# Kernel tuning notes

Hardware: AMD Instinct MI355X
Metric: run time of the kernel (lower is better)

Reference implementation:

```python
import jax, jax.numpy as jnp
import numpy as np

D = 256      # d_model
NH = 8       # num_heads
NP = 4       # n_points
H = 100      # feature map height (single level)
W = 100      # feature map width
B = 4
Q = H * W
S = H * W


def setup_inputs() -> dict:
    key = jax.random.key(0)
    ks = jax.random.split(key, 12)
    p = lambda k, shp, s=0.02: jax.random.normal(k, shp, jnp.float32) * s
    return {
        "hidden_states": jax.random.normal(ks[0], (B, Q, D), jnp.float32),
        "encoder_hidden_states": jax.random.normal(ks[1], (B, S, D), jnp.float32),
        "reference_points": jax.random.uniform(ks[2], (B, Q, 1, 2), jnp.float32),
        "spatial_shapes": jnp.array([[H, W]], dtype=jnp.int32),
        "W_off": p(ks[3], (NH * NP * 2, D)),
        "b_off": p(ks[4], (NH * NP * 2,), 0.5),
        "W_attn": p(ks[5], (NH * NP, D)),
        "b_attn": jnp.zeros((NH * NP,), jnp.float32),
        "W_val": p(ks[6], (D, D)),
        "b_val": jnp.zeros((D,), jnp.float32),
        "W_out": p(ks[7], (D, D)),
        "b_out": jnp.zeros((D,), jnp.float32),
    }


def _deform_attn(hidden_states, encoder_hidden_states, reference_points,
                 W_off, b_off, W_attn, b_attn, W_val, b_val, W_out, b_out):
    Bsz, Qn, Dm = hidden_states.shape
    d = Dm // NH

    # value projection -> [B, NH, S, d]
    value = (encoder_hidden_states @ W_val.T + b_val).reshape(Bsz, S, NH, d)
    vflat = value.transpose(0, 2, 1, 3).reshape(Bsz * NH, H * W, d)

    # sampling offsets [B,Q,NH,NP,2] (n_levels=1 squeezed)
    off = (hidden_states @ W_off.T + b_off).reshape(Bsz, Qn, NH, NP, 2)
    # attention weights softmax over (n_levels*n_points)=NP -> [B,Q,NH,NP]
    attn = jax.nn.softmax((hidden_states @ W_attn.T + b_attn).reshape(Bsz, Qn, NH, NP), axis=-1)

    # normalized sampling locations: ref + off / [W, H]
    normalizer = jnp.array([W, H], jnp.float32)
    # reference_points: [B,Q,1,2] (level dim) -> broadcast over heads/points
    loc = reference_points[:, :, None, 0, None, :] + off / normalizer  # [B,Q,NH,NP,2]

    # grid_sample semantics: grid = 2*loc - 1, align_corners=False, zeros padding
    gx = 2.0 * loc[..., 0] - 1.0
    gy = 2.0 * loc[..., 1] - 1.0
    x = ((gx + 1.0) * W - 1.0) * 0.5   # pixel coords [B,Q,NH,NP]
    y = ((gy + 1.0) * H - 1.0) * 0.5
    x0 = jnp.floor(x); y0 = jnp.floor(y)
    x1 = x0 + 1.0;     y1 = y0 + 1.0
    wx1 = x - x0; wx0 = 1.0 - wx1
    wy1 = y - y0; wy0 = 1.0 - wy1

    bh = jnp.arange(Bsz * NH)[:, None]

    def corner(xi, yi, wgt):
        valid = (xi >= 0) & (xi <= W - 1) & (yi >= 0) & (yi <= H - 1)
        xi_c = jnp.clip(xi, 0, W - 1).astype(jnp.int32)
        yi_c = jnp.clip(yi, 0, H - 1).astype(jnp.int32)
        idx = (yi_c * W + xi_c).transpose(0, 2, 1, 3).reshape(Bsz * NH, Qn * NP)
        g = vflat[bh, idx]  # [B*NH, Q*NP, d]
        wv = (wgt * valid.astype(wgt.dtype)).transpose(0, 2, 1, 3).reshape(Bsz * NH, Qn * NP, 1)
        return g * wv

    sampled = corner(x0, y0, wx0 * wy0)
    sampled = sampled + corner(x1, y0, wx1 * wy0)
    sampled = sampled + corner(x0, y1, wx0 * wy1)
    sampled = sampled + corner(x1, y1, wx1 * wy1)
    sampled = sampled.reshape(Bsz, NH, Qn, NP, d)

    out = jnp.einsum("bhqpd,bqhp->bqhd", sampled, attn).reshape(Bsz, Qn, Dm)
    return out @ W_out.T + b_out


def reference(hidden_states, encoder_hidden_states, reference_points, spatial_shapes,
              W_off, b_off, W_attn, b_attn, W_val, b_val, W_out, b_out):
    # spatial_shapes is static metadata (must equal [[H, W]]); shapes are baked in.
    return _deform_attn(hidden_states, encoder_hidden_states, reference_points,
                        W_off, b_off, W_attn, b_attn, W_val, b_val, W_out, b_out)
```

## Files before the change

kernel.cpp:

```cpp
#include <hip/hip_runtime.h>

constexpr int HH = 100;
constexpr int WW = 100;
constexpr int NH = 8;
constexpr int NP = 4;
constexpr int B  = 4;
constexpr int Q  = HH * WW;
constexpr int S  = Q;
constexpr int K  = 256;
constexpr int DH = 32;

typedef __attribute__((ext_vector_type(8))) short short8;
typedef __attribute__((ext_vector_type(4))) float f32x4;

struct ushort4_t { unsigned short x, y, z, w; };

__device__ inline unsigned short f2bf(float f) {
    unsigned u = __builtin_bit_cast(unsigned, f);
    u += 0x7fffu + ((u >> 16) & 1u);
    return (unsigned short)(u >> 16);
}
__device__ inline float bf2f(unsigned short h) {
    return __builtin_bit_cast(float, ((unsigned)h) << 16);
}

__device__ inline void lds_store16(short* base, int row, int kcol, short8 v) {
    const int idx = row * 64 + (kcol ^ ((row & 7) << 3));
    *reinterpret_cast<short8*>(&base[idx]) = v;
}
__device__ inline short8 lds_load16(const short* base, int row, int kcol) {
    const int idx = row * 64 + (kcol ^ ((row & 7) << 3));
    return *reinterpret_cast<const short8*>(&base[idx]);
}

__device__ inline short8 cvt8(float4 a, float4 b) {
    short8 r;
    r[0] = (short)f2bf(a.x); r[1] = (short)f2bf(a.y);
    r[2] = (short)f2bf(a.z); r[3] = (short)f2bf(a.w);
    r[4] = (short)f2bf(b.x); r[5] = (short)f2bf(b.y);
    r[6] = (short)f2bf(b.z); r[7] = (short)f2bf(b.w);
    return r;
}

template <int MODE, int NT>
__global__ __launch_bounds__(512) void gemm_mfma(
    const void* __restrict__ Ap, const float* __restrict__ W0,
    const float* __restrict__ W1, const float* __restrict__ b0,
    const float* __restrict__ b1, void* __restrict__ Cp, int N0)
{
    constexpr int BROWS = (NT + 63) / 64;

    __shared__ short As[64 * 64];
    __shared__ short Bs[NT * 64];

    const int tid  = threadIdx.x;
    const int m0   = blockIdx.x * 64;
    const int lane = tid & 63;
    const int w    = tid >> 6;
    const int l15  = lane & 15;
    const int l4   = lane >> 4;
    const int srow = tid >> 3;
    const int sk8  = (tid & 7) * 8;

    const int n_base = (MODE == 1) ? w * 16 : w * 32;
    constexpr int NF = (MODE == 1) ? 1 : 2;

    f32x4 acc[4][2];
#pragma unroll
    for (int i = 0; i < 4; ++i)
#pragma unroll
        for (int j = 0; j < 2; ++j)
            acc[i][j] = f32x4{0.f, 0.f, 0.f, 0.f};

    float4 fa0, fa1;
    short8 sa;
    float4 fb[BROWS][2];

    auto load_tile = [&](int k0) {
        if constexpr (MODE == 2) {
            const unsigned short* A = (const unsigned short*)Ap;
            sa = *reinterpret_cast<const short8*>(&A[(size_t)(m0 + srow) * K + k0 + sk8]);
        } else {
            const float* A = (const float*)Ap;
            const float* s = &A[(size_t)(m0 + srow) * K + k0 + sk8];
            fa0 = *reinterpret_cast<const float4*>(s);
            fa1 = *reinterpret_cast<const float4*>(s + 4);
        }
#pragma unroll
        for (int i = 0; i < BROWS; ++i) {
            const int row = srow + 64 * i;
            if ((NT % 64 == 0) || row < NT) {
                const float* s = (row < N0)
                    ? &W0[(size_t)row * K + k0 + sk8]
                    : &W1[(size_t)(row - N0) * K + k0 + sk8];
                fb[i][0] = *reinterpret_cast<const float4*>(s);
                fb[i][1] = *reinterpret_cast<const float4*>(s + 4);
            }
        }
    };
    auto write_lds = [&]() {
        if constexpr (MODE == 2) {
            lds_store16(As, srow, sk8, sa);
        } else {
            lds_store16(As, srow, sk8, cvt8(fa0, fa1));
        }
#pragma unroll
        for (int i = 0; i < BROWS; ++i) {
            const int row = srow + 64 * i;
            if ((NT % 64 == 0) || row < NT)
                lds_store16(Bs, row, sk8, cvt8(fb[i][0], fb[i][1]));
        }
    };

    load_tile(0);
    for (int k0 = 0; k0 < K; k0 += 64) {
        write_lds();
        __syncthreads();
        if (k0 + 64 < K) load_tile(k0 + 64);
        if (n_base < NT) {
#pragma unroll
            for (int kk = 0; kk < 2; ++kk) {
                const int kc = kk * 32 + l4 * 8;
                short8 a[4];
#pragma unroll
                for (int mf = 0; mf < 4; ++mf)
                    a[mf] = lds_load16(As, mf * 16 + l15, kc);
#pragma unroll
                for (int nf = 0; nf < NF; ++nf) {
                    const short8 bv = lds_load16(Bs, n_base + nf * 16 + l15, kc);
#pragma unroll
                    for (int mf = 0; mf < 4; ++mf)
                        acc[mf][nf] = __builtin_amdgcn_mfma_f32_16x16x32_bf16(
                            a[mf], bv, acc[mf][nf], 0, 0, 0);
                }
            }
        }
        __syncthreads();
    }

#pragma unroll
    for (int nf = 0; nf < NF; ++nf) {
        const int n = n_base + nf * 16 + l15;
        if (n >= NT) continue;
        const float bias = (n < N0) ? b0[n] : b1[n - N0];
#pragma unroll
        for (int mf = 0; mf < 4; ++mf) {
#pragma unroll
            for (int r = 0; r < 4; ++r) {
                const int m = m0 + mf * 16 + l4 * 4 + r;
                const float v = acc[mf][nf][r] + bias;
                if constexpr (MODE == 0) {
                    const int b = m / S, s = m - (m / S) * S;
                    const int h = n >> 5, dd = n & 31;
                    ((unsigned short*)Cp)[(((size_t)(b * NH + h)) * S + s) * DH + dd] = f2bf(v);
                } else if constexpr (MODE == 1) {
                    ((float*)Cp)[(size_t)m * 96 + n] = v;
                } else {
                    ((float*)Cp)[(size_t)m * 256 + n] = v;
                }
            }
        }
    }
}

__global__ __launch_bounds__(256) void sample_agg(
    const unsigned short* __restrict__ vflat,
    const float* __restrict__ proj,
    const float* __restrict__ ref,
    unsigned short* __restrict__ tmp)
{
    const int nblk = gridDim.x;
    const int cpx  = nblk >> 3;
    const int swz  = (blockIdx.x & 7) * cpx + (blockIdx.x >> 3);

    const int lg   = threadIdx.x >> 3;
    const int lane = threadIdx.x & 7;
    const int d0   = lane * 4;

    const int g  = swz * 32 + lg;
    const int q  = g % Q;
    const int bh = g / Q;
    const int b  = bh >> 3;
    const int h  = bh & 7;

    const size_t bq   = (size_t)b * Q + q;
    const float refx = ref[bq * 2 + 0];
    const float refy = ref[bq * 2 + 1];
    const float* pr = proj + bq * 96;

    float l[NP];
#pragma unroll
    for (int p = 0; p < NP; ++p) l[p] = pr[64 + h * 4 + p];
    const float mx = fmaxf(fmaxf(l[0], l[1]), fmaxf(l[2], l[3]));
    float e[NP];
    float esum = 0.f;
#pragma unroll
    for (int p = 0; p < NP; ++p) { e[p] = __expf(l[p] - mx); esum += e[p]; }
    const float inv = 1.f / esum;

    const unsigned short* vbase = vflat + (size_t)bh * (S * DH);

    int   cidx[NP][4];
    float cw[NP][4];
#pragma unroll
    for (int p = 0; p < NP; ++p) {
        const float ox = pr[h * 8 + p * 2 + 0];
        const float oy = pr[h * 8 + p * 2 + 1];
        const float x = (refx + ox * (1.0f / WW)) * WW - 0.5f;
        const float y = (refy + oy * (1.0f / HH)) * HH - 0.5f;
        const float x0f = floorf(x);
        const float y0f = floorf(y);
        const float wx1 = x - x0f, wx0 = 1.f - wx1;
        const float wy1 = y - y0f, wy0 = 1.f - wy1;
        const int x0 = (int)x0f;
        const int y0 = (int)y0f;
        const bool vx0 = (x0 >= 0) && (x0 <= WW - 1);
        const bool vx1 = (x0 + 1 >= 0) && (x0 + 1 <= WW - 1);
        const bool vy0 = (y0 >= 0) && (y0 <= HH - 1);
        const bool vy1 = (y0 + 1 >= 0) && (y0 + 1 <= HH - 1);
        const int xi0 = min(max(x0, 0), WW - 1);
        const int xi1 = min(max(x0 + 1, 0), WW - 1);
        const int yi0 = min(max(y0, 0), HH - 1);
        const int yi1 = min(max(y0 + 1, 0), HH - 1);
        const float ap = e[p] * inv;
        cw[p][0] = ap * wx0 * wy0 * ((vx0 && vy0) ? 1.f : 0.f);
        cw[p][1] = ap * wx1 * wy0 * ((vx1 && vy0) ? 1.f : 0.f);
        cw[p][2] = ap * wx0 * wy1 * ((vx0 && vy1) ? 1.f : 0.f);
        cw[p][3] = ap * wx1 * wy1 * ((vx1 && vy1) ? 1.f : 0.f);
        cidx[p][0] = (yi0 * WW + xi0) * DH + d0;
        cidx[p][1] = (yi0 * WW + xi1) * DH + d0;
        cidx[p][2] = (yi1 * WW + xi0) * DH + d0;
        cidx[p][3] = (yi1 * WW + xi1) * DH + d0;
    }

    float a0 = 0.f, a1 = 0.f, a2 = 0.f, a3 = 0.f;
#pragma unroll
    for (int p = 0; p < NP; ++p) {
#pragma unroll
        for (int c = 0; c < 4; ++c) {
            const ushort4_t v = *reinterpret_cast<const ushort4_t*>(&vbase[cidx[p][c]]);
            const float wgt = cw[p][c];
            a0 = fmaf(wgt, bf2f(v.x), a0);
            a1 = fmaf(wgt, bf2f(v.y), a1);
            a2 = fmaf(wgt, bf2f(v.z), a2);
            a3 = fmaf(wgt, bf2f(v.w), a3);
        }
    }

    ushort4_t o;
    o.x = f2bf(a0); o.y = f2bf(a1); o.z = f2bf(a2); o.w = f2bf(a3);
    *reinterpret_cast<ushort4_t*>(&tmp[bq * 256 + h * 32 + d0]) = o;
}

extern "C" void kernel_launch(void* const* d_in, const int* in_sizes, int n_in,
                              void* d_out, int out_size, void* d_ws, size_t ws_size,
                              hipStream_t stream)
{
    const float* hidden = (const float*)d_in[0];
    const float* enc    = (const float*)d_in[1];
    const float* refp   = (const float*)d_in[2];
    const float* W_off  = (const float*)d_in[4];
    const float* b_off  = (const float*)d_in[5];
    const float* W_attn = (const float*)d_in[6];
    const float* b_attn = (const float*)d_in[7];
    const float* W_val  = (const float*)d_in[8];
    const float* b_val  = (const float*)d_in[9];
    const float* W_out  = (const float*)d_in[10];
    const float* b_out  = (const float*)d_in[11];
    float* out = (float*)d_out;

    unsigned short* vflat = (unsigned short*)d_ws;
    float* proj = (float*)((char*)d_ws + (size_t)B * NH * S * DH * 2);
    unsigned short* tmp = (unsigned short*)((char*)proj + (size_t)B * Q * 96 * 4);

    const int M = B * Q;

    gemm_mfma<0, 256><<<M / 64, 512, 0, stream>>>(
        (const void*)enc, W_val, W_val, b_val, b_val, (void*)vflat, 256);

    gemm_mfma<1, 96><<<M / 64, 512, 0, stream>>>(
        (const void*)hidden, W_off, W_attn, b_off, b_attn, (void*)proj, 64);

    sample_agg<<<(B * NH * Q) / 32, 256, 0, stream>>>(vflat, proj, refp, tmp);

    gemm_mfma<2, 256><<<M / 64, 512, 0, stream>>>(
        (const void*)tmp, W_out, W_out, b_out, b_out, (void*)out, 256);
}
```

Baseline: 89.46 us.

## Rewrite GEMMs as persistent LDS-resident-weight kernels with bf16 weight preconversion

Adds a kernel that converts all weight matrices to bf16 once, then replaces the three tiled GEMM launches with persistent 1024-thread kernels. Each of these loads the full weight matrix into LDS once and loops over 32-row tiles of activations, prefetching the next tile. The offset/attention projection output is stored in fp16 instead of fp32 to halve its traffic. The sampling kernel now loads 8 channels per thread with 16-byte reads. Risks include lower occupancy from the large LDS footprint, serialized tile loops, and fp16 precision loss on the sampling offsets.

```diff
diff --git a/kernel.cpp b/kernel.cpp
--- a/kernel.cpp
+++ b/kernel.cpp
@@ -9,11 +9,13 @@
 constexpr int S  = Q;
 constexpr int K  = 256;
 constexpr int DH = 32;
+constexpr int M  = B * Q;
+constexpr int NTILES = M / 32;
 
 typedef __attribute__((ext_vector_type(8))) short short8;
 typedef __attribute__((ext_vector_type(4))) float f32x4;
 
-struct ushort4_t { unsigned short x, y, z, w; };
+struct __align__(8) ushort4_t { unsigned short x, y, z, w; };
 
 __device__ inline unsigned short f2bf(float f) {
     unsigned u = __builtin_bit_cast(unsigned, f);
@@ -23,14 +25,19 @@
 __device__ inline float bf2f(unsigned short h) {
     return __builtin_bit_cast(float, ((unsigned)h) << 16);
 }
-
-__device__ inline void lds_store16(short* base, int row, int kcol, short8 v) {
-    const int idx = row * 64 + (kcol ^ ((row & 7) << 3));
-    *reinterpret_cast<short8*>(&base[idx]) = v;
-}
-__device__ inline short8 lds_load16(const short* base, int row, int kcol) {
-    const int idx = row * 64 + (kcol ^ ((row & 7) << 3));
-    return *reinterpret_cast<const short8*>(&base[idx]);
+__device__ inline unsigned short f2h(float f) {
+    _Float16 h = (_Float16)f;
+    return __builtin_bit_cast(unsigned short, h);
+}
+__device__ inline float h2f(unsigned short u) {
+    return (float)__builtin_bit_cast(_Float16, u);
+}
+
+__device__ inline void lds_st16s(short* base, int row, int stride, int kcol, short8 v) {
+    *reinterpret_cast<short8*>(&base[row * stride + (kcol ^ ((row & 7) << 3))]) = v;
+}
+__device__ inline short8 lds_ld16s(const short* base, int row, int stride, int kcol) {
+    return *reinterpret_cast<const short8*>(&base[row * stride + (kcol ^ ((row & 7) << 3))]);
 }
 
 __device__ inline short8 cvt8(float4 a, float4 b) {
@@ -42,130 +49,155 @@
     return r;
 }
 
-template <int MODE, int NT>
-__global__ __launch_bounds__(512) void gemm_mfma(
-    const void* __restrict__ Ap, const float* __restrict__ W0,
-    const float* __restrict__ W1, const float* __restrict__ b0,
-    const float* __restrict__ b1, void* __restrict__ Cp, int N0)
-{
-    constexpr int BROWS = (NT + 63) / 64;
-
-    __shared__ short As[64 * 64];
-    __shared__ short Bs[NT * 64];
+__global__ __launch_bounds__(256) void preconv(
+    const float* __restrict__ wval, const float* __restrict__ woff,
+    const float* __restrict__ wattn, const float* __restrict__ wo,
+    unsigned short* __restrict__ wbf)
+{
+    const int i4 = (blockIdx.x * 256 + threadIdx.x) * 4;
+    const float* src;
+    if (i4 < 65536) {
+        src = wval + i4;
+    } else if (i4 < 90112) {
+        const int local = i4 - 65536;
+        src = (local < 16384) ? woff + local : wattn + (local - 16384);
+    } else {
+        src = wo + (i4 - 90112);
+    }
+    const float4 f = *reinterpret_cast<const float4*>(src);
+    ushort4_t o;
+    o.x = f2bf(f.x); o.y = f2bf(f.y); o.z = f2bf(f.z); o.w = f2bf(f.w);
+    *reinterpret_cast<ushort4_t*>(&wbf[i4]) = o;
+}
+
+__global__ __launch_bounds__(1024) void value_persist(
+    const float* __restrict__ enc, const unsigned short* __restrict__ wbf,
+    const float* __restrict__ bias, unsigned short* __restrict__ vflat)
+{
+    __shared__ short Bs[256 * 256];
+    __shared__ short As[32 * 256];
 
     const int tid  = threadIdx.x;
-    const int m0   = blockIdx.x * 64;
-    const int lane = tid & 63;
-    const int w    = tid >> 6;
-    const int l15  = lane & 15;
-    const int l4   = lane >> 4;
-    const int srow = tid >> 3;
-    const int sk8  = (tid & 7) * 8;
-
-    const int n_base = (MODE == 1) ? w * 16 : w * 32;
-    constexpr int NF = (MODE == 1) ? 1 : 2;
-
-    f32x4 acc[4][2];
-#pragma unroll
-    for (int i = 0; i < 4; ++i)
-#pragma unroll
-        for (int j = 0; j < 2; ++j)
-            acc[i][j] = f32x4{0.f, 0.f, 0.f, 0.f};
-
+    const int lane = tid & 63, w = tid >> 6;
+    const int l15  = lane & 15, l4 = lane >> 4;
+
+    const int arow = tid >> 5, ak = (tid & 31) * 8;
+
+    int t = blockIdx.x;
     float4 fa0, fa1;
-    short8 sa;
-    float4 fb[BROWS][2];
-
-    auto load_tile = [&](int k0) {
-        if constexpr (MODE == 2) {
-            const unsigned short* A = (const unsigned short*)Ap;
-            sa = *reinterpret_cast<const short8*>(&A[(size_t)(m0 + srow) * K + k0 + sk8]);
-        } else {
-            const float* A = (const float*)Ap;
-            const float* s = &A[(size_t)(m0 + srow) * K + k0 + sk8];
-            fa0 = *reinterpret_cast<const float4*>(s);
-            fa1 = *reinterpret_cast<const float4*>(s + 4);
-        }
-#pragma unroll
-        for (int i = 0; i < BROWS; ++i) {
-            const int row = srow + 64 * i;
-            if ((NT % 64 == 0) || row < NT) {
-                const float* s = (row < N0)
-                    ? &W0[(size_t)row * K + k0 + sk8]
-                    : &W1[(size_t)(row - N0) * K + k0 + sk8];
-                fb[i][0] = *reinterpret_cast<const float4*>(s);
-                fb[i][1] = *reinterpret_cast<const float4*>(s + 4);
+    auto lda = [&](int tt) {
+        const float* s = &enc[(size_t)(tt * 32 + arow) * K + ak];
+        fa0 = *reinterpret_cast<const float4*>(s);
+        fa1 = *reinterpret_cast<const float4*>(s + 4);
+    };
+    lda(t);
+
+    {
+        const int brow = tid >> 2, kb = (tid & 3) * 64;
+#pragma unroll
+        for (int c = 0; c < 8; ++c) {
+            short8 v = *reinterpret_cast<const short8*>(&wbf[brow * 256 + kb + c * 8]);
+            lds_st16s(Bs, brow, 256, kb + c * 8, v);
+        }
+    }
+
+    const int nb = w * 16;
+    const int n = nb + l15;
+    const float bv = bias[n];
+    const int h = n >> 5, dd = n & 31;
+
+    for (; t < NTILES; t += 256) {
+        lds_st16s(As, arow, 256, ak, cvt8(fa0, fa1));
+        __syncthreads();
+        if (t + 256 < NTILES) lda(t + 256);
+
+        f32x4 acc0 = {0.f, 0.f, 0.f, 0.f}, acc1 = {0.f, 0.f, 0.f, 0.f};
+#pragma unroll
+        for (int ks = 0; ks < 8; ++ks) {
+            const int kc = ks * 32 + l4 * 8;
+            const short8 bb = lds_ld16s(Bs, n, 256, kc);
+            const short8 a0 = lds_ld16s(As, l15, 256, kc);
+            const short8 a1 = lds_ld16s(As, 16 + l15, 256, kc);
+            acc0 = __builtin_amdgcn_mfma_f32_16x16x32_bf16(a0, bb, acc0, 0, 0, 0);
+            acc1 = __builtin_amdgcn_mfma_f32_16x16x32_bf16(a1, bb, acc1, 0, 0, 0);
+        }
+        const int m0 = t * 32;
+#pragma unroll
+        for (int r = 0; r < 4; ++r) {
+            int m = m0 + l4 * 4 + r;
+            int b_ = m / S, s_ = m - b_ * S;
+            vflat[(((size_t)(b_ * NH + h)) * S + s_) * DH + dd] = f2bf(acc0[r] + bv);
+            m += 16; b_ = m / S; s_ = m - b_ * S;
+            vflat[(((size_t)(b_ * NH + h)) * S + s_) * DH + dd] = f2bf(acc1[r] + bv);
+        }
+        __syncthreads();
+    }
+}
+
+__global__ __launch_bounds__(1024) void proj_persist(
+    const float* __restrict__ hidden, const unsigned short* __restrict__ wbf,
+    const float* __restrict__ boff, const float* __restrict__ battn,
+    unsigned short* __restrict__ proj)
+{
+    __shared__ short Bs[96 * 256];
+    __shared__ short As[32 * 256];
+
+    const int tid  = threadIdx.x;
+    const int lane = tid & 63, w = tid >> 6;
+    const int l15  = lane & 15, l4 = lane >> 4;
+
+    const int arow = tid >> 5, ak = (tid & 31) * 8;
+
+    int t = blockIdx.x;
+    float4 fa0, fa1;
+    auto lda = [&](int tt) {
+        const float* s = &hidden[(size_t)(tt * 32 + arow) * K + ak];
+        fa0 = *reinterpret_cast<const float4*>(s);
+        fa1 = *reinterpret_cast<const float4*>(s + 4);
+    };
+    lda(t);
+
+    {
+#pragma unroll
+        for (int j = 0; j < 3; ++j) {
+            const int ch = tid * 3 + j;
+            const int brow = ch >> 5, kc = (ch & 31) * 8;
+            short8 v = *reinterpret_cast<const short8*>(&wbf[brow * 256 + kc]);
+            lds_st16s(Bs, brow, 256, kc, v);
+        }
+    }
+
+    const int nf = w >> 1, mh = w & 1;
+    const int n = nf * 16 + l15;
+    const float bv = (w < 12) ? ((n < 64) ? boff[n] : battn[n - 64]) : 0.f;
+
+    for (; t < NTILES; t += 512) {
+        lds_st16s(As, arow, 256, ak, cvt8(fa0, fa1));
+        __syncthreads();
+        if (t + 512 < NTILES) lda(t + 512);
+
+        if (w < 12) {
+            f32x4 acc = {0.f, 0.f, 0.f, 0.f};
+#pragma unroll
+            for (int ks = 0; ks < 8; ++ks) {
+                const int kc = ks * 32 + l4 * 8;
+                const short8 bb = lds_ld16s(Bs, n, 256, kc);
+                const short8 a = lds_ld16s(As, mh * 16 + l15, 256, kc);
+                acc = __builtin_amdgcn_mfma_f32_16x16x32_bf16(a, bb, acc, 0, 0, 0);
             }
-        }
-    };
-    auto write_lds = [&]() {
-        if constexpr (MODE == 2) {
-            lds_store16(As, srow, sk8, sa);
-        } else {
-            lds_store16(As, srow, sk8, cvt8(fa0, fa1));
-        }
-#pragma unroll
-        for (int i = 0; i < BROWS; ++i) {
-            const int row = srow + 64 * i;
-            if ((NT % 64 == 0) || row < NT)
-                lds_store16(Bs, row, sk8, cvt8(fb[i][0], fb[i][1]));
-        }
-    };
-
-    load_tile(0);
-    for (int k0 = 0; k0 < K; k0 += 64) {
-        write_lds();
-        __syncthreads();
-        if (k0 + 64 < K) load_tile(k0 + 64);
-        if (n_base < NT) {
-#pragma unroll
-            for (int kk = 0; kk < 2; ++kk) {
-                const int kc = kk * 32 + l4 * 8;
-                short8 a[4];
-#pragma unroll
-                for (int mf = 0; mf < 4; ++mf)
-                    a[mf] = lds_load16(As, mf * 16 + l15, kc);
-#pragma unroll
-                for (int nf = 0; nf < NF; ++nf) {
-                    const short8 bv = lds_load16(Bs, n_base + nf * 16 + l15, kc);
-#pragma unroll
-                    for (int mf = 0; mf < 4; ++mf)
-                        acc[mf][nf] = __builtin_amdgcn_mfma_f32_16x16x32_bf16(
-                            a[mf], bv, acc[mf][nf], 0, 0, 0);
-                }
+#pragma unroll
+            for (int r = 0; r < 4; ++r) {
+                const int m = t * 32 + mh * 16 + l4 * 4 + r;
+                proj[(size_t)m * 96 + n] = f2h(acc[r] + bv);
             }
         }
         __syncthreads();
-    }
-
-#pragma unroll
-    for (int nf = 0; nf < NF; ++nf) {
-        const int n = n_base + nf * 16 + l15;
-        if (n >= NT) continue;
-        const float bias = (n < N0) ? b0[n] : b1[n - N0];
-#pragma unroll
-        for (int mf = 0; mf < 4; ++mf) {
-#pragma unroll
-            for (int r = 0; r < 4; ++r) {
-                const int m = m0 + mf * 16 + l4 * 4 + r;
-                const float v = acc[mf][nf][r] + bias;
-                if constexpr (MODE == 0) {
-                    const int b = m / S, s = m - (m / S) * S;
-                    const int h = n >> 5, dd = n & 31;
-                    ((unsigned short*)Cp)[(((size_t)(b * NH + h)) * S + s) * DH + dd] = f2bf(v);
-                } else if constexpr (MODE == 1) {
-                    ((float*)Cp)[(size_t)m * 96 + n] = v;
-                } else {
-                    ((float*)Cp)[(size_t)m * 256 + n] = v;
-                }
-            }
-        }
     }
 }
 
 __global__ __launch_bounds__(256) void sample_agg(
     const unsigned short* __restrict__ vflat,
-    const float* __restrict__ proj,
+    const unsigned short* __restrict__ proj,
     const float* __restrict__ ref,
     unsigned short* __restrict__ tmp)
 {
@@ -173,24 +205,24 @@
     const int cpx  = nblk >> 3;
     const int swz  = (blockIdx.x & 7) * cpx + (blockIdx.x >> 3);
 
-    const int lg   = threadIdx.x >> 3;
-    const int lane = threadIdx.x & 7;
-    const int d0   = lane * 4;
-
-    const int g  = swz * 32 + lg;
+    const int lg   = threadIdx.x >> 2;
+    const int lane = threadIdx.x & 3;
+    const int d0   = lane * 8;
+
+    const int g  = swz * 64 + lg;
     const int q  = g % Q;
     const int bh = g / Q;
     const int b  = bh >> 3;
     const int h  = bh & 7;
 
-    const size_t bq   = (size_t)b * Q + q;
+    const size_t bq = (size_t)b * Q + q;
     const float refx = ref[bq * 2 + 0];
     const float refy = ref[bq * 2 + 1];
-    const float* pr = proj + bq * 96;
+    const unsigned short* pr = proj + bq * 96;
 
     float l[NP];
 #pragma unroll
-    for (int p = 0; p < NP; ++p) l[p] = pr[64 + h * 4 + p];
+    for (int p = 0; p < NP; ++p) l[p] = h2f(pr[64 + h * 4 + p]);
     const float mx = fmaxf(fmaxf(l[0], l[1]), fmaxf(l[2], l[3]));
     float e[NP];
     float esum = 0.f;
@@ -204,20 +236,18 @@
     float cw[NP][4];
 #pragma unroll
     for (int p = 0; p < NP; ++p) {
-        const float ox = pr[h * 8 + p * 2 + 0];
-        const float oy = pr[h * 8 + p * 2 + 1];
-        const float x = (refx + ox * (1.0f / WW)) * WW - 0.5f;
-        const float y = (refy + oy * (1.0f / HH)) * HH - 0.5f;
-        const float x0f = floorf(x);
-        const float y0f = floorf(y);
+        const float ox = h2f(pr[h * 8 + p * 2 + 0]);
+        const float oy = h2f(pr[h * 8 + p * 2 + 1]);
+        const float x = fmaf(refx, (float)WW, ox) - 0.5f;
+        const float y = fmaf(refy, (float)HH, oy) - 0.5f;
+        const float x0f = floorf(x), y0f = floorf(y);
         const float wx1 = x - x0f, wx0 = 1.f - wx1;
         const float wy1 = y - y0f, wy0 = 1.f - wy1;
-        const int x0 = (int)x0f;
-        const int y0 = (int)y0f;
-        const bool vx0 = (x0 >= 0) && (x0 <= WW - 1);
-        const bool vx1 = (x0 + 1 >= 0) && (x0 + 1 <= WW - 1);
-        const bool vy0 = (y0 >= 0) && (y0 <= HH - 1);
-        const bool vy1 = (y0 + 1 >= 0) && (y0 + 1 <= HH - 1);
+        const int x0 = (int)x0f, y0 = (int)y0f;
+        const bool vx0 = (x0 >= 0) && (x0 < WW);
+        const bool vx1 = (x0 + 1 >= 0) && (x0 + 1 < WW);
+        const bool vy0 = (y0 >= 0) && (y0 < HH);
+        const bool vy1 = (y0 + 1 >= 0) && (y0 + 1 < HH);
         const int xi0 = min(max(x0, 0), WW - 1);
         const int xi1 = min(max(x0 + 1, 0), WW - 1);
         const int yi0 = min(max(y0, 0), HH - 1);
@@ -233,23 +263,83 @@
         cidx[p][3] = (yi1 * WW + xi1) * DH + d0;
     }
 
-    float a0 = 0.f, a1 = 0.f, a2 = 0.f, a3 = 0.f;
+    float o[8];
+#pragma unroll
+    for (int j = 0; j < 8; ++j) o[j] = 0.f;
 #pragma unroll
     for (int p = 0; p < NP; ++p) {
 #pragma unroll
         for (int c = 0; c < 4; ++c) {
-            const ushort4_t v = *reinterpret_cast<const ushort4_t*>(&vbase[cidx[p][c]]);
+            const short8 v = *reinterpret_cast<const short8*>(&vbase[cidx[p][c]]);
             const float wgt = cw[p][c];
-            a0 = fmaf(wgt, bf2f(v.x), a0);
-            a1 = fmaf(wgt, bf2f(v.y), a1);
-            a2 = fmaf(wgt, bf2f(v.z), a2);
-            a3 = fmaf(wgt, bf2f(v.w), a3);
-        }
-    }
-
-    ushort4_t o;
-    o.x = f2bf(a0); o.y = f2bf(a1); o.z = f2bf(a2); o.w = f2bf(a3);
-    *reinterpret_cast<ushort4_t*>(&tmp[bq * 256 + h * 32 + d0]) = o;
+#pragma unroll
+            for (int j = 0; j < 8; ++j)
+                o[j] = fmaf(wgt, bf2f((unsigned short)v[j]), o[j]);
+        }
+    }
+
+    short8 ov;
+#pragma unroll
+    for (int j = 0; j < 8; ++j) ov[j] = (short)f2bf(o[j]);
+    *reinterpret_cast<short8*>(&tmp[bq * 256 + h * 32 + d0]) = ov;
+}
+
+__global__ __launch_bounds__(1024) void out_persist(
+    const unsigned short* __restrict__ tmp, const unsigned short* __restrict__ wbf,
+    const float* __restrict__ bias, float* __restrict__ out)
+{
+    __shared__ short Bs[256 * 256];
+    __shared__ short As[32 * 256];
+
+    const int tid  = threadIdx.x;
+    const int lane = tid & 63, w = tid >> 6;
+    const int l15  = lane & 15, l4 = lane >> 4;
+
+    const int arow = tid >> 5, ak = (tid & 31) * 8;
+
+    int t = blockIdx.x;
+    short8 sa;
+    auto lda = [&](int tt) {
+        sa = *reinterpret_cast<const short8*>(&tmp[(size_t)(tt * 32 + arow) * K + ak]);
+    };
+    lda(t);
+
+    {
+        const int brow = tid >> 2, kb = (tid & 3) * 64;
+#pragma unroll
+        for (int c = 0; c < 8; ++c) {
+            short8 v = *reinterpret_cast<const short8*>(&wbf[brow * 256 + kb + c * 8]);
+            lds_st16s(Bs, brow, 256, kb + c * 8, v);
+        }
+    }
+
+    const int n = w * 16 + l15;
+    const float bv = bias[n];
+
+    for (; t < NTILES; t += 256) {
+        lds_st16s(As, arow, 256, ak, sa);
+        __syncthreads();
+        if (t + 256 < NTILES) lda(t + 256);
+
+        f32x4 acc0 = {0.f, 0.f, 0.f, 0.f}, acc1 = {0.f, 0.f, 0.f, 0.f};
+#pragma unroll
+        for (int ks = 0; ks < 8; ++ks) {
+            const int kc = ks * 32 + l4 * 8;
+            const short8 bb = lds_ld16s(Bs, n, 256, kc);
+            const short8 a0 = lds_ld16s(As, l15, 256, kc);
+            const short8 a1 = lds_ld16s(As, 16 + l15, 256, kc);
+            acc0 = __builtin_amdgcn_mfma_f32_16x16x32_bf16(a0, bb, acc0, 0, 0, 0);
+            acc1 = __builtin_amdgcn_mfma_f32_16x16x32_bf16(a1, bb, acc1, 0, 0, 0);
+        }
+        const int m0 = t * 32;
+#pragma unroll
+        for (int r = 0; r < 4; ++r) {
+            const int m = m0 + l4 * 4 + r;
+            out[(size_t)m * K + n] = acc0[r] + bv;
+            out[(size_t)(m + 16) * K + n] = acc1[r] + bv;
+        }
+        __syncthreads();
+    }
 }
 
 extern "C" void kernel_launch(void* const* d_in, const int* in_sizes, int n_in,
@@ -270,19 +360,17 @@
     float* out = (float*)d_out;
 
     unsigned short* vflat = (unsigned short*)d_ws;
-    float* proj = (float*)((char*)d_ws + (size_t)B * NH * S * DH * 2);
-    unsigned short* tmp = (unsigned short*)((char*)proj + (size_t)B * Q * 96 * 4);
-
-    const int M = B * Q;
-
-    gemm_mfma<0, 256><<<M / 64, 512, 0, stream>>>(
-        (const void*)enc, W_val, W_val, b_val, b_val, (void*)vflat, 256);
-
-    gemm_mfma<1, 96><<<M / 64, 512, 0, stream>>>(
-        (const void*)hidden, W_off, W_attn, b_off, b_attn, (void*)proj, 64);
-
-    sample_agg<<<(B * NH * Q) / 32, 256, 0, stream>>>(vflat, proj, refp, tmp);
-
-    gemm_mfma<2, 256><<<M / 64, 512, 0, stream>>>(
-        (const void*)tmp, W_out, W_out, b_out, b_out, (void*)out, 256);
-}
+    unsigned short* tmp   = vflat + (size_t)10240000;
+    unsigned short* proj  = tmp + (size_t)10240000;
+    unsigned short* wbf   = proj + (size_t)3840000;
+
+    preconv<<<152, 256, 0, stream>>>(W_val, W_off, W_attn, W_out, wbf);
+
+    value_persist<<<256, 1024, 0, stream>>>(enc, wbf, b_val, vflat);
+
+    proj_persist<<<512, 1024, 0, stream>>>(hidden, wbf + 65536, b_off, b_attn, proj);
+
+    sample_agg<<<5000, 256, 0, stream>>>(vflat, proj, refp, tmp);
+
+    out_persist<<<256, 1024, 0, stream>>>(tmp, wbf + 90112, b_out, out);
+}
```

Result: faster. 80.17 us (-10.4%).
